# Performance work log

Measured on AMD Instinct MI355X. Metric: run time of the kernel, lower is better.

## Reference

```python
import jax, jax.numpy as jnp
import numpy as np

B, N_PER, D = 128, 512, 128        # graphs, nodes per graph, feature width
N = B * N_PER                      # 65536 total nodes
E = 524288                         # total edges (avg degree 8)
KS = (410, 328, 263)               # ceil(0.8*512), ceil(0.8*410), ceil(0.8*328)


def setup_inputs() -> dict:
    key = jax.random.key(0)
    ks = jax.random.split(key, 20)
    p = lambda k, shape: jax.random.normal(k, shape, jnp.float32) * 0.05
    rng = np.random.default_rng(0)
    g = rng.integers(0, B, size=E)
    s = rng.integers(0, N_PER, size=E)
    t = rng.integers(0, N_PER, size=E)
    edge_index = jnp.asarray(np.stack([g * N_PER + s, g * N_PER + t]).astype(np.int32))
    inp = {
        'x': jax.random.normal(ks[0], (N, 1, D), jnp.float32),
        'edge_index': edge_index,
    }
    i = 1
    for l in (1, 2, 3):
        inp[f'conv{l}_wl'] = p(ks[i], (D, D)); i += 1   # SAGEConv lin_l (neighbors) weight
        inp[f'conv{l}_bl'] = p(ks[i], (D,));  i += 1   # SAGEConv lin_l bias
        inp[f'conv{l}_wr'] = p(ks[i], (D, D)); i += 1   # SAGEConv lin_r (root) weight
        inp[f'pool{l}_w'] = p(ks[i], (D,));   i += 1   # TopKPooling score vector
    inp['lin1_w'] = p(ks[13], (128, 256)); inp['lin1_b'] = p(ks[14], (128,))
    inp['lin2_w'] = p(ks[15], (64, 128));  inp['lin2_b'] = p(ks[16], (64,))
    inp['lin3_w'] = p(ks[17], (1, 64));    inp['lin3_b'] = p(ks[18], (1,))
    return inp


def _sage(x, node_mask, src, dst, wl, bl, wr):
    # SAGEConv, mean aggregation: lin_l(mean_{j->i} x_j) + lin_r(x_i)
    em = (node_mask[src] & node_mask[dst]).astype(x.dtype)   # [E] valid-edge mask
    msum = jax.ops.segment_sum(x[src] * em[:, None], dst, num_segments=N)
    deg = jax.ops.segment_sum(em, dst, num_segments=N)
    mean = msum / jnp.maximum(deg, 1.0)[:, None]
    return mean @ wl.T + bl + x @ wr.T


def _topk_pool(x, node_mask, w, k):
    # TopKPooling: score = x.w/||w||; keep top-k per graph; gate kept x by tanh(score)
    score = (x @ w) / (jnp.linalg.norm(w) + 1e-16)           # [N]
    score = jnp.where(node_mask, score, -jnp.inf)
    _, idx = jax.lax.top_k(score.reshape(B, N_PER), k)       # [B, k] within-graph ids
    nm = jnp.zeros((B, N_PER), bool).at[jnp.arange(B)[:, None], idx].set(True).reshape(-1)
    x = jnp.where(nm[:, None], x * jnp.tanh(score)[:, None], 0.0)
    return x, nm


def _readout(x, node_mask, k):
    # cat([global_max_pool, global_mean_pool]) over the k surviving nodes per graph
    xb = x.reshape(B, N_PER, -1)
    mb = node_mask.reshape(B, N_PER, 1)
    gmax = jnp.max(jnp.where(mb, xb, -jnp.inf), axis=1)
    gmean = jnp.sum(jnp.where(mb, xb, 0.0), axis=1) / k
    return jnp.concatenate([gmax, gmean], axis=1)            # [B, 2D]


def _forward(edge_index, x, conv1_wl, conv1_bl, conv1_wr, pool1_w,
             conv2_wl, conv2_bl, conv2_wr, pool2_w,
             conv3_wl, conv3_bl, conv3_wr, pool3_w,
             lin1_w, lin1_b, lin2_w, lin2_b, lin3_w, lin3_b):
    src, dst = edge_index[0], edge_index[1]
    h = x[:, 0, :]                                           # x.squeeze(1) -> [N, D]
    nm = jnp.ones((N,), bool)
    layers = ((conv1_wl, conv1_bl, conv1_wr, pool1_w),
              (conv2_wl, conv2_bl, conv2_wr, pool2_w),
              (conv3_wl, conv3_bl, conv3_wr, pool3_w))
    reads = []
    for (wl, bl, wr, pw), k in zip(layers, KS):
        h = jax.nn.relu(_sage(h, nm, src, dst, wl, bl, wr))
        h, nm = _topk_pool(h, nm, pw, k)
        reads.append(_readout(h, nm, float(k)))
    z = reads[0] + reads[1] + reads[2]                       # [B, 256]
    z = jax.nn.relu(z @ lin1_w.T + lin1_b)
    z = jax.nn.relu(z @ lin2_w.T + lin2_b)
    # dropout p=0.5 is a no-op at eval time
    return jax.nn.sigmoid(z @ lin3_w.T + lin3_b)[:, 0]       # [B]


def reference(x, edge_index, conv1_wl, conv1_bl, conv1_wr, pool1_w,
              conv2_wl, conv2_bl, conv2_wr, pool2_w,
              conv3_wl, conv3_bl, conv3_wr, pool3_w,
              lin1_w, lin1_b, lin2_w, lin2_b, lin3_w, lin3_b):
    return _forward(edge_index, x, conv1_wl, conv1_bl, conv1_wr, pool1_w,
                    conv2_wl, conv2_bl, conv2_wr, pool2_w,
                    conv3_wl, conv3_bl, conv3_wr, pool3_w,
                    lin1_w, lin1_b, lin2_w, lin2_b, lin3_w, lin3_b)
```

## Files before the change

kernel.cpp:

```cpp
#include <hip/hip_runtime.h>
#include <math.h>

#define NND 65536
#define NPER 512
#define NGR 128
#define DD 128
#define NED 524288

typedef __attribute__((ext_vector_type(8))) short short8;
typedef __attribute__((ext_vector_type(4))) float f32x4;

__device__ __forceinline__ unsigned short f2b(float f) {
  unsigned u = __float_as_uint(f);
  return (unsigned short)((u + 0x7FFFu + ((u >> 16) & 1u)) >> 16);
}
__device__ __forceinline__ float b2f(unsigned short h) {
  return __uint_as_float(((unsigned)h) << 16);
}


__global__ __launch_bounds__(256) void init_prepw_kernel(
    int* __restrict__ counts, float2* __restrict__ tm,
    const float* __restrict__ wl0, const float* __restrict__ wr0,
    const float* __restrict__ wl1, const float* __restrict__ wr1,
    const float* __restrict__ wl2, const float* __restrict__ wr2,
    unsigned short* __restrict__ Whi, unsigned short* __restrict__ Wlo) {
  const int bid = blockIdx.x;
  if (bid < 256) {
    int i = bid * 256 + threadIdx.x;
    counts[i] = 0;
    tm[i] = make_float2(1.f, 1.f);
    return;
  }
  const float* wls[3] = {wl0, wl1, wl2};
  const float* wrs[3] = {wr0, wr1, wr2};
  int e = (bid - 256) * 256 + threadIdx.x;
  int l = e >> 15;
  int o = e & 32767;
  int j = o & 7;
  int lane = (o >> 3) & 63;
  int nt = (o >> 9) & 7;
  int kc = o >> 12;
  int li = lane & 15, q = lane >> 4;
  int n = nt * 16 + li;
  int k = kc * 32 + q * 8 + j;
  const float* src = (k < 128) ? wls[l] : wrs[l];
  float v = src[n * DD + (k & 127)];
  unsigned short hi = f2b(v);
  float lo = v - b2f(hi);
  Whi[e] = hi;
  Wlo[e] = f2b(lo);
}

__global__ __launch_bounds__(256) void hist_kernel(const int* __restrict__ ei,
                                                   int* __restrict__ counts) {
  int e = blockIdx.x * 256 + threadIdx.x;
  atomicAdd(&counts[ei[NED + e]], 1);
}


__global__ __launch_bounds__(256) void scan1_kernel(const int* __restrict__ counts,
                                                    int* __restrict__ csum) {
  __shared__ int ws[4];
  const int b = blockIdx.x;
  const int t = threadIdx.x;
  const int4 v = ((const int4*)(counts + b * 1024))[t];
  int s = v.x + v.y + v.z + v.w;
#pragma unroll
  for (int o = 32; o > 0; o >>= 1) s += __shfl_down(s, o);
  if ((t & 63) == 0) ws[t >> 6] = s;
  __syncthreads();
  if (t == 0) csum[b] = ws[0] + ws[1] + ws[2] + ws[3];
}

__global__ __launch_bounds__(256) void scan2_kernel(const int* __restrict__ counts,
                                                    const int* __restrict__ csum,
                                                    int* __restrict__ off,
                                                    int* __restrict__ cursor) {
  __shared__ int s_part[256];
  __shared__ int s_base;
  const int b = blockIdx.x;
  const int t = threadIdx.x;
  const int4 v = ((const int4*)(counts + b * 1024))[t];
  const int s = v.x + v.y + v.z + v.w;
  s_part[t] = s;
  if (t < 64) {
    int val = (t < b) ? csum[t] : 0;
#pragma unroll
    for (int o = 32; o > 0; o >>= 1) val += __shfl_down(val, o);
    if (t == 0) s_base = val;
  }
  __syncthreads();
  for (int d = 1; d < 256; d <<= 1) {
    int val = (t >= d) ? s_part[t - d] : 0;
    __syncthreads();
    s_part[t] += val;
    __syncthreads();
  }
  const int excl = s_base + ((t == 0) ? 0 : s_part[t - 1]);
  int4 o4;
  o4.x = excl;
  o4.y = excl + v.x;
  o4.z = o4.y + v.y;
  o4.w = o4.z + v.z;
  ((int4*)(off + b * 1024))[t] = o4;
  ((int4*)(cursor + b * 1024))[t] = o4;
  if (b == 0 && t == 0) off[NND] = NED;
}

__global__ __launch_bounds__(256) void scatter_kernel(const int* __restrict__ ei,
                                                      int* __restrict__ cursor,
                                                      int* __restrict__ ssrc) {
  int e = blockIdx.x * 256 + threadIdx.x;
  int dst = ei[NED + e];
  int pos = atomicAdd(&cursor[dst], 1);
  ssrc[pos] = ei[e];
}


template <int CM>
__global__ __launch_bounds__(1024) void agg_kernel_t(const float* __restrict__ x,
                                                     const float2* __restrict__ tm,
                                                     const int* __restrict__ off,
                                                     const int* __restrict__ ssrc,
                                                     unsigned short* __restrict__ mhi,
                                                     unsigned short* __restrict__ mlo) {
  __shared__ float xs[NPER * 64];
  __shared__ float2 tms[NPER];
  __shared__ int soff[NPER + 1];
  const int b = blockIdx.x;
  const int g = b >> 1;
  const int colbase = (b & 1) << 6;
  const int tid = threadIdx.x;
  const int lane = tid & 63;
  const int w = tid >> 6;
  const int nbase = g * NPER;

  {
    const int row = tid >> 4;
    const int c4 = (tid & 15) << 2;
#pragma unroll
    for (int r = 0; r < NPER; r += 64) {
      const float4 v =
          *(const float4*)(x + (size_t)(nbase + row + r) * DD + colbase + c4);
      *(float4*)(xs + (row + r) * 64 + c4) = v;
    }
  }
  if (CM) {
    if (tid < NPER) tms[tid] = tm[nbase + tid];
  }
  if (tid < NPER + 1) soff[tid] = off[nbase + tid];
  __syncthreads();

  const float* xl = xs + lane;
  for (int i = 0; i < 32; ++i) {
    const int n = w * 32 + i;
    if (CM && tms[n].x == 0.f) continue;
    const int beg = soff[n];
    const int end = soff[n + 1];
    float acc = 0.f;
    int deg = 0;
    for (int base = beg; base < end; base += 64) {
      const int cnt = min(64, end - base);
      int sv = 0;
      float tv = 0.f;
      int live = 0;
      if (lane < cnt) {
        sv = (ssrc[base + lane] & (NPER - 1)) << 6;
        if (CM) {
          const float2 mt = tms[sv >> 6];
          live = (mt.x != 0.f);
          tv = mt.y;
        }
      }
      if (CM)
        deg += (int)__popcll(__ballot(live));
      else
        deg += cnt;
      int j = 0;
      if (CM) {
        for (; j + 3 < cnt; j += 4) {
          const int s0 = __shfl(sv, j), s1 = __shfl(sv, j + 1);
          const int s2 = __shfl(sv, j + 2), s3 = __shfl(sv, j + 3);
          const float t0 = __shfl(tv, j), t1 = __shfl(tv, j + 1);
          const float t2 = __shfl(tv, j + 2), t3 = __shfl(tv, j + 3);
          const float v0 = xl[s0], v1 = xl[s1], v2 = xl[s2], v3 = xl[s3];
          acc += v0 * t0;
          acc += v1 * t1;
          acc += v2 * t2;
          acc += v3 * t3;
        }
        for (; j < cnt; ++j) {
          const int s = __shfl(sv, j);
          const float t = __shfl(tv, j);
          acc += xl[s] * t;
        }
      } else {
        for (; j + 3 < cnt; j += 4) {
          const int s0 = __shfl(sv, j), s1 = __shfl(sv, j + 1);
          const int s2 = __shfl(sv, j + 2), s3 = __shfl(sv, j + 3);
          const float v0 = xl[s0], v1 = xl[s1], v2 = xl[s2], v3 = xl[s3];
          acc += v0;
          acc += v1;
          acc += v2;
          acc += v3;
        }
        for (; j < cnt; ++j) {
          const int s = __shfl(sv, j);
          acc += xl[s];
        }
      }
    }
    const float m = acc * (1.f / (float)max(deg, 1));
    const unsigned short hv = f2b(m);
    const unsigned short lv = f2b(m - b2f(hv));
    const size_t ad = (size_t)(nbase + n) * DD + colbase + lane;
    mhi[ad] = hv;
    mlo[ad] = lv;
  }
}


#define GBM 64

template <int SCALE>
__global__ __launch_bounds__(256) void gemm_kernel_t(
    const unsigned short* __restrict__ Amh, const unsigned short* __restrict__ Aml,
    const float* __restrict__ Ax, const float2* __restrict__ tmp,
    const unsigned short* __restrict__ Whi, const unsigned short* __restrict__ Wlo,
    const float* __restrict__ bias, const float* __restrict__ pw,
    float* __restrict__ outp, float* __restrict__ sraw) {
  __shared__ short Ah[4096];
  __shared__ short Al[4096];
  __shared__ float s_sp[4][GBM];
  const int tid = threadIdx.x;
  const int wv = tid >> 6;
  const int lane = tid & 63;
  const int q = lane >> 4;
  const int li = lane & 15;
  const int row0 = blockIdx.x * GBM;

  int sdst[2];
#pragma unroll
  for (int i = 0; i < 2; ++i) {
    const int id = tid + i * 256;
    const int r = id >> 3;
    const int kb = (id & 7) << 2;
    sdst[i] = ((r >> 4) * 64 + (kb >> 3) * 16 + (r & 15)) * 8 + (kb & 7);
  }

  f32x4 acc[4][2];
#pragma unroll
  for (int m = 0; m < 4; ++m)
#pragma unroll
    for (int n = 0; n < 2; ++n) acc[m][n] = (f32x4){0.f, 0.f, 0.f, 0.f};

  float4 pa[2];
  ushort4 pmh[2], pml[2];
  short8 pbh[2], pbl[2];

#define LOADA(KC)                                                                      \
  {                                                                                    \
    if ((KC) < 4) {                                                                    \
      const int cb = (KC)*32;                                                          \
      _Pragma("unroll") for (int i = 0; i < 2; ++i) {                                  \
        const int id = tid + i * 256;                                                  \
        const size_t ga = (size_t)(row0 + (id >> 3)) * DD + cb + ((id & 7) << 2);      \
        pmh[i] = *(const ushort4*)(Amh + ga);                                          \
        pml[i] = *(const ushort4*)(Aml + ga);                                          \
      }                                                                                \
    } else {                                                                           \
      const int cb = ((KC)&3) * 32;                                                    \
      _Pragma("unroll") for (int i = 0; i < 2; ++i) {                                  \
        const int id = tid + i * 256;                                                  \
        pa[i] = *(const float4*)(Ax + (size_t)(row0 + (id >> 3)) * DD + cb + ((id & 7) << 2)); \
        if (SCALE) {                                                                   \
          const float tt = tmp[row0 + (id >> 3)].y;                                    \
          pa[i].x *= tt; pa[i].y *= tt; pa[i].z *= tt; pa[i].w *= tt;                  \
        }                                                                              \
      }                                                                                \
    }                                                                                  \
  }
#define LOADB(KC)                                                                      \
  {                                                                                    \
    _Pragma("unroll") for (int n = 0; n < 2; ++n) {                                    \
      const int ga = (((KC)*8 + wv * 2 + n) * 64 + lane) * 8;                          \
      pbh[n] = *(const short8*)(Whi + ga);                                             \
      pbl[n] = *(const short8*)(Wlo + ga);                                             \
    }                                                                                  \
  }
#define STAGE(KC)                                                                      \
  {                                                                                    \
    short* Adh = Ah + ((KC)&1) * 2048;                                                 \
    short* Adl = Al + ((KC)&1) * 2048;                                                 \
    if ((KC) < 4) {                                                                    \
      _Pragma("unroll") for (int i = 0; i < 2; ++i) {                                  \
        *(ushort4*)(Adh + sdst[i]) = pmh[i];                                           \
        *(ushort4*)(Adl + sdst[i]) = pml[i];                                           \
      }                                                                                \
    } else {                                                                           \
      _Pragma("unroll") for (int i = 0; i < 2; ++i) {                                  \
        ushort4 hv, lv;                                                                \
        hv.x = f2b(pa[i].x); lv.x = f2b(pa[i].x - b2f(hv.x));                          \
        hv.y = f2b(pa[i].y); lv.y = f2b(pa[i].y - b2f(hv.y));                          \
        hv.z = f2b(pa[i].z); lv.z = f2b(pa[i].z - b2f(hv.z));                          \
        hv.w = f2b(pa[i].w); lv.w = f2b(pa[i].w - b2f(hv.w));                          \
        *(ushort4*)(Adh + sdst[i]) = hv;                                               \
        *(ushort4*)(Adl + sdst[i]) = lv;                                               \
      }                                                                                \
    }                                                                                  \
  }

  LOADA(0) LOADB(0)
  STAGE(0)
  LOADA(1)

#pragma unroll
  for (int kc = 0; kc < 8; ++kc) {
    short8 bh[2], bl[2];
    bh[0] = pbh[0]; bh[1] = pbh[1];
    bl[0] = pbl[0]; bl[1] = pbl[1];
    __syncthreads();
    short8 ah[4], al[4];
    const short* Ash = Ah + (kc & 1) * 2048;
    const short* Asl = Al + (kc & 1) * 2048;
#pragma unroll
    for (int m = 0; m < 4; ++m) {
      ah[m] = *(const short8*)(Ash + (m * 64 + lane) * 8);
      al[m] = *(const short8*)(Asl + (m * 64 + lane) * 8);
    }
    switch (kc) {
      case 0: STAGE(1) LOADB(1) LOADA(2) break;
      case 1: STAGE(2) LOADB(2) LOADA(3) break;
      case 2: STAGE(3) LOADB(3) LOADA(4) break;
      case 3: STAGE(4) LOADB(4) LOADA(5) break;
      case 4: STAGE(5) LOADB(5) LOADA(6) break;
      case 5: STAGE(6) LOADB(6) LOADA(7) break;
      case 6: STAGE(7) LOADB(7) break;
      default: break;
    }
#pragma unroll
    for (int m = 0; m < 4; ++m)
#pragma unroll
      for (int n = 0; n < 2; ++n) {
        acc[m][n] = __builtin_amdgcn_mfma_f32_16x16x32_bf16(ah[m], bh[n], acc[m][n], 0, 0, 0);
        acc[m][n] = __builtin_amdgcn_mfma_f32_16x16x32_bf16(ah[m], bl[n], acc[m][n], 0, 0, 0);
        acc[m][n] = __builtin_amdgcn_mfma_f32_16x16x32_bf16(al[m], bh[n], acc[m][n], 0, 0, 0);
      }
  }
#undef LOADA
#undef LOADB
#undef STAGE

  const int c0 = wv * 32 + li;
  const int c1 = wv * 32 + 16 + li;
  const float b0 = bias[c0], b1 = bias[c1];
  const float p0 = pw[c0], p1 = pw[c1];
  float sp[16];
#pragma unroll
  for (int m = 0; m < 4; ++m) {
#pragma unroll
    for (int i = 0; i < 4; ++i) {
      const int r = row0 + m * 16 + q * 4 + i;
      const float v0 = fmaxf(acc[m][0][i] + b0, 0.f);
      const float v1 = fmaxf(acc[m][1][i] + b1, 0.f);
      outp[(size_t)r * DD + c0] = v0;
      outp[(size_t)r * DD + c1] = v1;
      sp[m * 4 + i] = v0 * p0 + v1 * p1;
    }
  }
#pragma unroll
  for (int e = 0; e < 16; ++e) {
    sp[e] += __shfl_xor(sp[e], 1);
    sp[e] += __shfl_xor(sp[e], 2);
    sp[e] += __shfl_xor(sp[e], 4);
    sp[e] += __shfl_xor(sp[e], 8);
  }
  if (li == 0) {
#pragma unroll
    for (int e = 0; e < 16; ++e) s_sp[wv][(e >> 2) * 16 + q * 4 + (e & 3)] = sp[e];
  }
  __syncthreads();
  if (tid < GBM)
    sraw[row0 + tid] = s_sp[0][tid] + s_sp[1][tid] + s_sp[2][tid] + s_sp[3][tid];
}


__global__ __launch_bounds__(256) void pool_kernel(const float* __restrict__ h,
                                                   const float* __restrict__ sraw,
                                                   const float* __restrict__ pw,
                                                   const float2* __restrict__ tmP,
                                                   float2* __restrict__ tmN,
                                                   float* __restrict__ zp,
                                                   const int kk) {
  __shared__ float s_sc[NPER];
  __shared__ float s_t[128];
  __shared__ unsigned char s_sel[128];
  __shared__ int s_rk[256];
  __shared__ float4 red4[512];
  __shared__ float s_norm;
  const int b = blockIdx.x;
  const int g = b >> 2;
  const int q = b & 3;
  const int tid = threadIdx.x;
  const int lane = tid & 63;

  if (tid < 64) {
    const float v0 = pw[lane], v1 = pw[lane + 64];
    float p = v0 * v0 + v1 * v1;
#pragma unroll
    for (int o = 32; o > 0; o >>= 1) p += __shfl_down(p, o);
    if (lane == 0) s_norm = 1.f / (sqrtf(p) + 1e-16f);
  }
  __syncthreads();
  const float inv_norm = s_norm;
#pragma unroll
  for (int i = 0; i < 2; ++i) {
    const int n = tid + i * 256;
    const int node = g * NPER + n;
    s_sc[n] = (tmP[node].x != 0.f) ? sraw[node] * inv_norm : -INFINITY;
  }
  __syncthreads();

  {
    const int n = q * 128 + (tid & 127);
    const int jb = (tid >> 7) * 256;
    const float s = s_sc[n];
    int rank = 0;
    for (int j = jb; j < jb + 256; ++j) {
      const float sj = s_sc[j];
      rank += (sj > s || (sj == s && j < n)) ? 1 : 0;
    }
    s_rk[tid] = rank;
  }
  __syncthreads();
  if (tid < 128) {
    const int n = q * 128 + tid;
    const int rank = s_rk[tid] + s_rk[tid + 128];
    const int sel = (rank < kk) ? 1 : 0;
    const float s = s_sc[n];
    const float t = sel ? tanhf(s) : 0.f;
    tmN[g * NPER + n] = make_float2(sel ? 1.f : 0.f, t);
    s_sel[tid] = (unsigned char)sel;
    s_t[tid] = t;
  }
  __syncthreads();

  const int c = tid & 31;
  const int r = tid >> 5;
  float4 pmax = make_float4(-INFINITY, -INFINITY, -INFINITY, -INFINITY);
  float4 psum = make_float4(0.f, 0.f, 0.f, 0.f);
  const size_t nbase = (size_t)g * NPER + q * 128;
  const float4* h4 = (const float4*)h;
  for (int i = 0; i < 16; ++i) {
    const int nl = r + 8 * i;
    if (s_sel[nl]) {
      float4 v = h4[(nbase + nl) * 32 + c];
      const float t = s_t[nl];
      v.x *= t; v.y *= t; v.z *= t; v.w *= t;
      pmax.x = fmaxf(pmax.x, v.x);
      pmax.y = fmaxf(pmax.y, v.y);
      pmax.z = fmaxf(pmax.z, v.z);
      pmax.w = fmaxf(pmax.w, v.w);
      psum.x += v.x; psum.y += v.y; psum.z += v.z; psum.w += v.w;
    }
  }
  red4[r * 32 + c] = pmax;
  red4[256 + r * 32 + c] = psum;
  __syncthreads();
  if (tid < 32) {
    float4 m = red4[tid];
    float4 sm = red4[256 + tid];
#pragma unroll
    for (int rr = 1; rr < 8; ++rr) {
      const float4 a = red4[rr * 32 + tid];
      const float4 s2 = red4[256 + rr * 32 + tid];
      m.x = fmaxf(m.x, a.x); m.y = fmaxf(m.y, a.y);
      m.z = fmaxf(m.z, a.z); m.w = fmaxf(m.w, a.w);
      sm.x += s2.x; sm.y += s2.y; sm.z += s2.z; sm.w += s2.w;
    }
    *(float4*)(zp + (size_t)b * 256 + tid * 4) = m;
    *(float4*)(zp + (size_t)b * 256 + 128 + tid * 4) = sm;
  }
}


__global__ __launch_bounds__(128) void mlp_kernel(const float* __restrict__ zpart,
                                                  const float* __restrict__ w1,
                                                  const float* __restrict__ b1,
                                                  const float* __restrict__ w2,
                                                  const float* __restrict__ b2,
                                                  const float* __restrict__ w3,
                                                  const float* __restrict__ b3,
                                                  float* __restrict__ out,
                                                  const float ik0, const float ik1,
                                                  const float ik2) {
  __shared__ float z[256];
  __shared__ float h1[128];
  __shared__ float h2[64];
  const int g = blockIdx.x;
  const int t = threadIdx.x;
  const float iks[3] = {ik0, ik1, ik2};
  float zmax = 0.f, zmean = 0.f;
#pragma unroll
  for (int l = 0; l < 3; ++l) {
    const float* zp = zpart + ((size_t)l * 512 + g * 4) * 256;
    zmax += fmaxf(fmaxf(zp[t], zp[256 + t]), fmaxf(zp[512 + t], zp[768 + t]));
    zmean += (zp[128 + t] + zp[384 + t] + zp[640 + t] + zp[896 + t]) * iks[l];
  }
  z[t] = zmax;
  z[128 + t] = zmean;
  __syncthreads();
  float a = b1[t];
  for (int k = 0; k < 256; ++k) a = fmaf(z[k], w1[t * 256 + k], a);
  h1[t] = fmaxf(a, 0.f);
  __syncthreads();
  if (t < 64) {
    float a2 = b2[t];
    for (int k = 0; k < 128; ++k) a2 = fmaf(h1[k], w2[t * 128 + k], a2);
    h2[t] = fmaxf(a2, 0.f);
  }
  __syncthreads();
  if (t == 0) {
    float a3 = b3[0];
    for (int k = 0; k < 64; ++k) a3 = fmaf(h2[k], w3[k], a3);
    out[g] = 1.f / (1.f + expf(-a3));
  }
}


extern "C" void kernel_launch(void* const* d_in, const int* in_sizes, int n_in,
                              void* d_out, int out_size, void* d_ws, size_t ws_size,
                              hipStream_t stream) {
  (void)in_sizes; (void)n_in; (void)out_size; (void)ws_size;
  const float* x_in = (const float*)d_in[0];
  const int* ei = (const int*)d_in[1];
  const float* wl[3] = {(const float*)d_in[2], (const float*)d_in[6], (const float*)d_in[10]};
  const float* cbl[3] = {(const float*)d_in[3], (const float*)d_in[7], (const float*)d_in[11]};
  const float* wr[3] = {(const float*)d_in[4], (const float*)d_in[8], (const float*)d_in[12]};
  const float* pw[3] = {(const float*)d_in[5], (const float*)d_in[9], (const float*)d_in[13]};
  const float* l1w = (const float*)d_in[14];
  const float* l1b = (const float*)d_in[15];
  const float* l2w = (const float*)d_in[16];
  const float* l2b = (const float*)d_in[17];
  const float* l3w = (const float*)d_in[18];
  const float* l3b = (const float*)d_in[19];
  float* out = (float*)d_out;

  char* w = (char*)d_ws;
  int* counts = (int*)(w + 0 * (1 << 20));
  int* off = (int*)(w + 1 * (1 << 20));
  int* csum = (int*)(w + 1 * (1 << 20) + (1 << 19));
  int* cursor = (int*)(w + 2 * (1 << 20));
  float* sraw = (float*)(w + 2 * (1 << 20));
  float2* tmA = (float2*)(w + 3 * (1 << 20));
  float2* tmB = (float2*)(w + 3 * (1 << 20) + (1 << 19));
  float* zpart = (float*)(w + 4 * (1 << 20));
  unsigned short* Whi = (unsigned short*)(w + 5 * (1 << 20) + (1 << 19));
  unsigned short* Wlo = (unsigned short*)(w + 5 * (1 << 20) + 3 * (1 << 18));
  int* ssrc = (int*)(w + 6 * (1 << 20));
  unsigned short* mhi = (unsigned short*)(w + (size_t)8 * (1 << 20));
  unsigned short* mlo = (unsigned short*)(w + (size_t)24 * (1 << 20));
  float* hA = (float*)(w + (size_t)40 * (1 << 20));
  float* hB = (float*)(w + (size_t)72 * (1 << 20));

  init_prepw_kernel<<<640, 256, 0, stream>>>(counts, tmA, wl[0], wr[0], wl[1], wr[1],
                                             wl[2], wr[2], Whi, Wlo);
  hist_kernel<<<NED / 256, 256, 0, stream>>>(ei, counts);
  scan1_kernel<<<64, 256, 0, stream>>>(counts, csum);
  scan2_kernel<<<64, 256, 0, stream>>>(counts, csum, off, cursor);
  scatter_kernel<<<NED / 256, 256, 0, stream>>>(ei, cursor, ssrc);

  const int ks[3] = {410, 328, 263};
  const float* xl = x_in;
  float* houts[3] = {hA, hB, hA};
  float2* tprev[3] = {tmA, tmB, tmA};
  float2* tnext[3] = {tmB, tmA, tmB};
  for (int l = 0; l < 3; ++l) {
    float* hout = houts[l];
    if (l == 0) {
      agg_kernel_t<0><<<NGR * 2, 1024, 0, stream>>>(xl, tprev[l], off, ssrc, mhi, mlo);
      gemm_kernel_t<0><<<NND / GBM, 256, 0, stream>>>(mhi, mlo, xl, tprev[l],
                                                      Whi + (size_t)l * 32768,
                                                      Wlo + (size_t)l * 32768, cbl[l], pw[l],
                                                      hout, sraw);
    } else {
      agg_kernel_t<1><<<NGR * 2, 1024, 0, stream>>>(xl, tprev[l], off, ssrc, mhi, mlo);
      gemm_kernel_t<1><<<NND / GBM, 256, 0, stream>>>(mhi, mlo, xl, tprev[l],
                                                      Whi + (size_t)l * 32768,
                                                      Wlo + (size_t)l * 32768, cbl[l], pw[l],
                                                      hout, sraw);
    }
    pool_kernel<<<NGR * 4, 256, 0, stream>>>(hout, sraw, pw[l], tprev[l], tnext[l],
                                             zpart + (size_t)l * 512 * 256, ks[l]);
    xl = hout;
  }
  mlp_kernel<<<NGR, 128, 0, stream>>>(zpart, l1w, l1b, l2w, l2b, l3w, l3b, out,
                                      1.f / 410.f, 1.f / 328.f, 1.f / 263.f);
}
```

Before: 405.3 us.

## Gather neighbor features from global memory in aggregation, precompute per-edge gates

The aggregation kernel no longer stages each graph's 512x64 feature slab in LDS. It now uses 256-thread blocks where each wave handles 8 destination nodes across all 128 columns, reading source rows straight from global or L2 as float2. Block ids are mapped so that all blocks of one graph land on the same XCD, which keeps reuse in L2. A new pe_kernel precomputes per-edge gate values and a 64-bit live mask per 64-edge chunk, so the aggregation loop no longer looks these up in a node table. This trades LDS staging and low occupancy (1024-thread blocks with 128KB+ of LDS) for more parallelism, at the cost of an extra kernel launch and more global traffic per layer.

```diff
diff --git a/kernel.cpp b/kernel.cpp
--- a/kernel.cpp
+++ b/kernel.cpp
@@ -118,105 +118,131 @@
 }
 
 
+__global__ __launch_bounds__(256) void pe_kernel(const int* __restrict__ ssrc,
+                                                 const float2* __restrict__ tm,
+                                                 float* __restrict__ pet,
+                                                 unsigned long long* __restrict__ plive) {
+  const int e = blockIdx.x * 256 + threadIdx.x;
+  const int s = ssrc[e];
+  const float2 mt = tm[s];
+  const int lv = (mt.x != 0.f) ? 1 : 0;
+  pet[e] = lv ? mt.y : 0.f;
+  const unsigned long long bl = __ballot(lv);
+  if ((threadIdx.x & 63) == 0) plive[e >> 6] = bl;
+}
+
+
 template <int CM>
-__global__ __launch_bounds__(1024) void agg_kernel_t(const float* __restrict__ x,
-                                                     const float2* __restrict__ tm,
-                                                     const int* __restrict__ off,
-                                                     const int* __restrict__ ssrc,
-                                                     unsigned short* __restrict__ mhi,
-                                                     unsigned short* __restrict__ mlo) {
-  __shared__ float xs[NPER * 64];
-  __shared__ float2 tms[NPER];
-  __shared__ int soff[NPER + 1];
-  const int b = blockIdx.x;
-  const int g = b >> 1;
-  const int colbase = (b & 1) << 6;
-  const int tid = threadIdx.x;
-  const int lane = tid & 63;
-  const int w = tid >> 6;
-  const int nbase = g * NPER;
-
-  {
-    const int row = tid >> 4;
-    const int c4 = (tid & 15) << 2;
-#pragma unroll
-    for (int r = 0; r < NPER; r += 64) {
-      const float4 v =
-          *(const float4*)(x + (size_t)(nbase + row + r) * DD + colbase + c4);
-      *(float4*)(xs + (row + r) * 64 + c4) = v;
-    }
-  }
-  if (CM) {
-    if (tid < NPER) tms[tid] = tm[nbase + tid];
-  }
-  if (tid < NPER + 1) soff[tid] = off[nbase + tid];
-  __syncthreads();
-
-  const float* xl = xs + lane;
-  for (int i = 0; i < 32; ++i) {
-    const int n = w * 32 + i;
-    if (CM && tms[n].x == 0.f) continue;
-    const int beg = soff[n];
-    const int end = soff[n + 1];
-    float acc = 0.f;
-    int deg = 0;
-    for (int base = beg; base < end; base += 64) {
-      const int cnt = min(64, end - base);
-      int sv = 0;
-      float tv = 0.f;
-      int live = 0;
-      if (lane < cnt) {
-        sv = (ssrc[base + lane] & (NPER - 1)) << 6;
+__global__ __launch_bounds__(256) void agg_kernel_t(
+    const float* __restrict__ x, const float2* __restrict__ tm,
+    const int* __restrict__ off, const int* __restrict__ ssrc,
+    const float* __restrict__ pet, const unsigned long long* __restrict__ plive,
+    unsigned short* __restrict__ mhi, unsigned short* __restrict__ mlo) {
+  const int wave = threadIdx.x >> 6;
+  const int lane = threadIdx.x & 63;
+  const int ll = lane * 2;
+  const int bid = blockIdx.x;
+  const int xcd = bid & 7;
+  const int idx = bid >> 3;
+  const int graph = xcd * 16 + (idx >> 4);
+  const int within = idx & 15;
+  const int d0 = graph * NPER + within * 32 + wave * 8;
+
+  int offv = 0;
+  if (lane < 9) offv = off[d0 + lane];
+  float deadv = 1.f;
+  if (CM && lane < 8) deadv = tm[d0 + lane].x;
+  int begs[8], ends[8];
+  float dd[8];
+#pragma unroll
+  for (int d = 0; d < 8; ++d) {
+    begs[d] = __shfl(offv, d);
+    ends[d] = __shfl(offv, d + 1);
+    dd[d] = CM ? __shfl(deadv, d) : 1.f;
+  }
+  const int b0 = begs[0];
+  const int e8 = ends[7];
+
+  float2 acc[8];
+  int deg[8];
+#pragma unroll
+  for (int d = 0; d < 8; ++d) {
+    acc[d] = make_float2(0.f, 0.f);
+    deg[d] = 0;
+  }
+
+  for (int wbase = b0 & ~63; wbase < e8; wbase += 64) {
+    const int sv = ssrc[wbase + lane];
+    float tv = 0.f;
+    unsigned long long lm = 0;
+    if (CM) {
+      tv = pet[wbase + lane];
+      lm = plive[wbase >> 6];
+    }
+#pragma unroll
+    for (int d = 0; d < 8; ++d) {
+      if (CM && dd[d] == 0.f) continue;
+      const int lo = max(begs[d], wbase);
+      const int hi = min(ends[d], wbase + 64);
+      if (lo >= hi) continue;
+      const int j0 = lo - wbase;
+      const int j1 = hi - wbase;
+      if (CM) {
+        const unsigned long long wm =
+            (((j1 == 64) ? ~0ull : ((1ull << j1) - 1)) & ~((1ull << j0) - 1));
+        deg[d] += (int)__popcll(lm & wm);
+      } else {
+        deg[d] += j1 - j0;
+      }
+      int j = j0;
+      for (; j + 3 < j1; j += 4) {
+        const int s0 = __shfl(sv, j), s1 = __shfl(sv, j + 1);
+        const int s2 = __shfl(sv, j + 2), s3 = __shfl(sv, j + 3);
+        const float2 v0 = *(const float2*)(x + (size_t)s0 * DD + ll);
+        const float2 v1 = *(const float2*)(x + (size_t)s1 * DD + ll);
+        const float2 v2 = *(const float2*)(x + (size_t)s2 * DD + ll);
+        const float2 v3 = *(const float2*)(x + (size_t)s3 * DD + ll);
         if (CM) {
-          const float2 mt = tms[sv >> 6];
-          live = (mt.x != 0.f);
-          tv = mt.y;
+          const float t0 = __shfl(tv, j), t1 = __shfl(tv, j + 1);
+          const float t2 = __shfl(tv, j + 2), t3 = __shfl(tv, j + 3);
+          acc[d].x += v0.x * t0; acc[d].y += v0.y * t0;
+          acc[d].x += v1.x * t1; acc[d].y += v1.y * t1;
+          acc[d].x += v2.x * t2; acc[d].y += v2.y * t2;
+          acc[d].x += v3.x * t3; acc[d].y += v3.y * t3;
+        } else {
+          acc[d].x += v0.x; acc[d].y += v0.y;
+          acc[d].x += v1.x; acc[d].y += v1.y;
+          acc[d].x += v2.x; acc[d].y += v2.y;
+          acc[d].x += v3.x; acc[d].y += v3.y;
         }
       }
-      if (CM)
-        deg += (int)__popcll(__ballot(live));
-      else
-        deg += cnt;
-      int j = 0;
-      if (CM) {
-        for (; j + 3 < cnt; j += 4) {
-          const int s0 = __shfl(sv, j), s1 = __shfl(sv, j + 1);
-          const int s2 = __shfl(sv, j + 2), s3 = __shfl(sv, j + 3);
-          const float t0 = __shfl(tv, j), t1 = __shfl(tv, j + 1);
-          const float t2 = __shfl(tv, j + 2), t3 = __shfl(tv, j + 3);
-          const float v0 = xl[s0], v1 = xl[s1], v2 = xl[s2], v3 = xl[s3];
-          acc += v0 * t0;
-          acc += v1 * t1;
-          acc += v2 * t2;
-          acc += v3 * t3;
-        }
-        for (; j < cnt; ++j) {
-          const int s = __shfl(sv, j);
+      for (; j < j1; ++j) {
+        const int s = __shfl(sv, j);
+        const float2 v = *(const float2*)(x + (size_t)s * DD + ll);
+        if (CM) {
           const float t = __shfl(tv, j);
-          acc += xl[s] * t;
-        }
-      } else {
-        for (; j + 3 < cnt; j += 4) {
-          const int s0 = __shfl(sv, j), s1 = __shfl(sv, j + 1);
-          const int s2 = __shfl(sv, j + 2), s3 = __shfl(sv, j + 3);
-          const float v0 = xl[s0], v1 = xl[s1], v2 = xl[s2], v3 = xl[s3];
-          acc += v0;
-          acc += v1;
-          acc += v2;
-          acc += v3;
-        }
-        for (; j < cnt; ++j) {
-          const int s = __shfl(sv, j);
-          acc += xl[s];
+          acc[d].x += v.x * t;
+          acc[d].y += v.y * t;
+        } else {
+          acc[d].x += v.x;
+          acc[d].y += v.y;
         }
       }
     }
-    const float m = acc * (1.f / (float)max(deg, 1));
-    const unsigned short hv = f2b(m);
-    const unsigned short lv = f2b(m - b2f(hv));
-    const size_t ad = (size_t)(nbase + n) * DD + colbase + lane;
-    mhi[ad] = hv;
-    mlo[ad] = lv;
+  }
+
+#pragma unroll
+  for (int d = 0; d < 8; ++d) {
+    if (CM && dd[d] == 0.f) continue;
+    const float inv = 1.f / (float)max(deg[d], 1);
+    const float mx = acc[d].x * inv;
+    const float my = acc[d].y * inv;
+    ushort2 hv, lv;
+    hv.x = f2b(mx); lv.x = f2b(mx - b2f(hv.x));
+    hv.y = f2b(my); lv.y = f2b(my - b2f(hv.y));
+    const size_t ad = (size_t)(d0 + d) * DD + ll;
+    *(ushort2*)(mhi + ad) = hv;
+    *(ushort2*)(mlo + ad) = lv;
   }
 }
 
@@ -563,6 +589,8 @@
   unsigned short* mlo = (unsigned short*)(w + (size_t)24 * (1 << 20));
   float* hA = (float*)(w + (size_t)40 * (1 << 20));
   float* hB = (float*)(w + (size_t)72 * (1 << 20));
+  float* pet = (float*)(w + (size_t)104 * (1 << 20));
+  unsigned long long* plive = (unsigned long long*)(w + (size_t)107 * (1 << 20));
 
   init_prepw_kernel<<<640, 256, 0, stream>>>(counts, tmA, wl[0], wr[0], wl[1], wr[1],
                                              wl[2], wr[2], Whi, Wlo);
@@ -579,13 +607,16 @@
   for (int l = 0; l < 3; ++l) {
     float* hout = houts[l];
     if (l == 0) {
-      agg_kernel_t<0><<<NGR * 2, 1024, 0, stream>>>(xl, tprev[l], off, ssrc, mhi, mlo);
+      agg_kernel_t<0><<<2048, 256, 0, stream>>>(xl, tprev[l], off, ssrc, pet, plive,
+                                                mhi, mlo);
       gemm_kernel_t<0><<<NND / GBM, 256, 0, stream>>>(mhi, mlo, xl, tprev[l],
                                                       Whi + (size_t)l * 32768,
                                                       Wlo + (size_t)l * 32768, cbl[l], pw[l],
                                                       hout, sraw);
     } else {
-      agg_kernel_t<1><<<NGR * 2, 1024, 0, stream>>>(xl, tprev[l], off, ssrc, mhi, mlo);
+      pe_kernel<<<NED / 256, 256, 0, stream>>>(ssrc, tprev[l], pet, plive);
+      agg_kernel_t<1><<<2048, 256, 0, stream>>>(xl, tprev[l], off, ssrc, pet, plive,
+                                                mhi, mlo);
       gemm_kernel_t<1><<<NND / GBM, 256, 0, stream>>>(mhi, mlo, xl, tprev[l],
                                                       Whi + (size_t)l * 32768,
                                                       Wlo + (size_t)l * 32768, cbl[l], pw[l],
```

New measurement: 381.0 us. -6.0%, faster.
